# Optimization experiments

Hardware: AMD Instinct MI355X
Metric: run time of the kernel (lower is better)

## Reference

```python
import jax, jax.numpy as jnp
import numpy as np

HID = 1          # hidden_size
LAYERS = 10      # num_layers
SCALE = 60.0     # range_adjusted


def _lstm_cell(x, h, c, W_ih, W_hh, b):
    # x: [B, in], h/c: [B, HID], W_ih: [4*HID, in], W_hh: [4*HID, HID], b: [4*HID]
    g = x @ W_ih.T + h @ W_hh.T + b  # [B, 4*HID], torch gate order i,f,g,o
    i = jax.nn.sigmoid(g[:, 0:HID])
    f = jax.nn.sigmoid(g[:, HID:2 * HID])
    gg = jnp.tanh(g[:, 2 * HID:3 * HID])
    o = jax.nn.sigmoid(g[:, 3 * HID:4 * HID])
    c_new = f * c + i * gg
    h_new = o * jnp.tanh(c_new)
    return h_new, c_new


def setup_inputs() -> dict:
    key = jax.random.key(0)
    ks = jax.random.split(key, 9)
    B, T, D = 4096, 512, 32
    state = jax.random.normal(ks[0], (B, T, D), jnp.float32)
    # torch LSTM init: uniform(-1/sqrt(hidden), 1/sqrt(hidden)) = uniform(-1, 1) since HID=1
    u = lambda k, shape: jax.random.uniform(k, shape, jnp.float32, -1.0, 1.0)
    W_ih0 = u(ks[1], (4 * HID, D))            # layer 0 input weights
    W_hh0 = u(ks[2], (4 * HID, HID))
    b0 = u(ks[3], (4 * HID,)) + u(ks[4], (4 * HID,))  # b_ih + b_hh fused
    W_ih_r = u(ks[5], (LAYERS - 1, 4 * HID, HID))      # layers 1..9 input size = HID
    W_hh_r = u(ks[6], (LAYERS - 1, 4 * HID, HID))
    b_r = u(ks[7], (LAYERS - 1, 4 * HID)) + u(ks[8], (LAYERS - 1, 4 * HID))
    return {"state": state, "W_ih0": W_ih0, "W_hh0": W_hh0, "b0": b0,
            "W_ih_r": W_ih_r, "W_hh_r": W_hh_r, "b_r": b_r}


def reference(state, W_ih0, W_hh0, b0, W_ih_r, W_hh_r, b_r):
    B, T, D = state.shape
    h0 = jnp.zeros((LAYERS, B, HID), state.dtype)
    c0 = jnp.zeros_like(h0)

    def step(carry, x_t):  # x_t: [B, D]
        h, c = carry
        hs, cs = [], []
        hh, cc = _lstm_cell(x_t, h[0], c[0], W_ih0, W_hh0, b0)
        hs.append(hh); cs.append(cc)
        for l in range(LAYERS - 1):  # fixed small layer loop
            hh, cc = _lstm_cell(hh, h[l + 1], c[l + 1], W_ih_r[l], W_hh_r[l], b_r[l])
            hs.append(hh); cs.append(cc)
        return (jnp.stack(hs), jnp.stack(cs)), hh  # hh: top-layer output [B, HID]

    _, ys = jax.lax.scan(step, (h0, c0), jnp.swapaxes(state, 0, 1))  # ys: [T, B, HID]
    lstm_out = jnp.swapaxes(ys, 0, 1)  # [B, T, HID]
    return jax.nn.sigmoid(lstm_out) * SCALE
```

## Files before the change

kernel.cpp:

```cpp
#include <hip/hip_runtime.h>

#define BB 4096
#define TT 512
#define DD 32
#define NL 10
#define PH 8
#define PHASES 66

static constexpr float L2E = 1.4426950408889634f;

typedef float f4 __attribute__((ext_vector_type(4)));

__device__ __forceinline__ float fexp2(float x) { return __builtin_amdgcn_exp2f(x); }
__device__ __forceinline__ float frcp(float x)  { return __builtin_amdgcn_rcpf(x); }
__device__ __forceinline__ float fmed3(float x, float a, float b) {
    return __builtin_amdgcn_fmed3f(x, a, b);
}

__device__ __forceinline__ float dpp_shr1(float x) {
    int r = __builtin_amdgcn_update_dpp(0, __float_as_int(x), 0x111, 0xF, 0xF, true);
    return __int_as_float(r);
}

template<int CTRL>
__device__ __forceinline__ float dpp_add(float x) {
    return x + __int_as_float(__builtin_amdgcn_update_dpp(
        0, __float_as_int(x), CTRL, 0xF, 0xF, true));
}
#define DPP_XOR1 0xB1
#define DPP_XOR2 0x4E
#define DPP_ROR4 0x124

__global__ __launch_bounds__(64) void k_fused(
    const float* __restrict__ x, const float* __restrict__ Wih0,
    const float* __restrict__ Whh0, const float* __restrict__ b0,
    const float* __restrict__ Wihr, const float* __restrict__ Whhr,
    const float* __restrict__ br, float* __restrict__ out)
{
    __shared__ float4 gbuf[2][4][PH + 1];

    const int lane = threadIdx.x & 63;
    const int blk  = blockIdx.x;

    const int pg = lane >> 3;
    const int pc = lane & 7;
    const f4 pw0 = *(const f4*)(Wih0 + 0 * DD + pc * 4);
    const f4 pw1 = *(const f4*)(Wih0 + 1 * DD + pc * 4);
    const f4 pw2 = *(const f4*)(Wih0 + 2 * DD + pc * 4);
    const f4 pw3 = *(const f4*)(Wih0 + 3 * DD + pc * 4);
    const float pb0 = b0[0], pb1 = b0[1], pb2 = b0[2], pb3 = b0[3];

    const int cidx = lane >> 4;
    const int l = lane & 15;
    const int chain = blk * 4 + cidx;
    const float sk0 = -L2E, sk1 = -L2E, sk2 = -2.f * L2E, sk3 = -L2E;
    const bool isl0 = (l == 0), isl9 = (l == NL - 1);
    const int li = (l >= 1 && l <= 9) ? (l - 1) : 0;

    float wi0 = 0, wi1 = 0, wi2 = 0, wi3 = 0;
    float wh0, wh1, wh2, wh3;
    float bb0 = 0, bb1 = 0, bb2 = 0, bb3 = 0;
    if (isl0) {
        wh0 = sk0 * Whh0[0]; wh1 = sk1 * Whh0[1];
        wh2 = sk2 * Whh0[2]; wh3 = sk3 * Whh0[3];
    } else {
        const float* pi = Wihr + li * 4;
        const float* ph = Whhr + li * 4;
        const float* pb = br   + li * 4;
        wi0 = sk0 * pi[0]; wi1 = sk1 * pi[1]; wi2 = sk2 * pi[2]; wi3 = sk3 * pi[3];
        wh0 = sk0 * ph[0]; wh1 = sk1 * ph[1]; wh2 = sk2 * ph[2]; wh3 = sk3 * ph[3];
        bb0 = sk0 * pb[0]; bb1 = sk1 * pb[1]; bb2 = sk2 * pb[2]; bb3 = sk3 * pb[3];
    }

    float* outp = out + (size_t)chain * TT;
    const float c2 = 2.f * L2E;
    float h = 0.f, cs = 0.f;
    float o0 = 0.f, o1 = 0.f, o2 = 0.f, o3 = 0.f;

    const float* xb = x + (size_t)blk * 4 * TT * DD;

    f4 VA0, VA1, VA2, VA3, VB0, VB1, VB2, VB3;

    auto LOADV = [&](f4& v0, f4& v1, f4& v2, f4& v3, int p) {
        int t = p * PH + pg; t = t < TT ? t : TT - 1;
        const float* base = xb + (size_t)t * DD + pc * 4;
        v0 = __builtin_nontemporal_load((const f4*)(base + 0 * TT * DD));
        v1 = __builtin_nontemporal_load((const f4*)(base + 1 * TT * DD));
        v2 = __builtin_nontemporal_load((const f4*)(base + 2 * TT * DD));
        v3 = __builtin_nontemporal_load((const f4*)(base + 3 * TT * DD));
    };

    auto PROD1 = [&](const f4 v, int ci, int slot) {
        float p0 = v.x * pw0.x + v.y * pw0.y + v.z * pw0.z + v.w * pw0.w;
        float p1 = v.x * pw1.x + v.y * pw1.y + v.z * pw1.z + v.w * pw1.w;
        float p2 = v.x * pw2.x + v.y * pw2.y + v.z * pw2.z + v.w * pw2.w;
        float p3 = v.x * pw3.x + v.y * pw3.y + v.z * pw3.z + v.w * pw3.w;
        p0 = dpp_add<DPP_XOR1>(p0); p1 = dpp_add<DPP_XOR1>(p1);
        p2 = dpp_add<DPP_XOR1>(p2); p3 = dpp_add<DPP_XOR1>(p3);
        p0 = dpp_add<DPP_XOR2>(p0); p1 = dpp_add<DPP_XOR2>(p1);
        p2 = dpp_add<DPP_XOR2>(p2); p3 = dpp_add<DPP_XOR2>(p3);
        p0 = dpp_add<DPP_ROR4>(p0); p1 = dpp_add<DPP_ROR4>(p1);
        p2 = dpp_add<DPP_ROR4>(p2); p3 = dpp_add<DPP_ROR4>(p3);
        if (pc == 0) {
            float4 o;
            o.x = -L2E * (p0 + pb0);
            o.y = -L2E * (p1 + pb1);
            o.z = -2.f * L2E * (p2 + pb2);
            o.w = -L2E * (p3 + pb3);
            gbuf[slot][ci][pg] = o;
        }
    };

    auto READR = [&](float4* R, int slot) {
        if (isl0) {
#pragma unroll
            for (int j = 0; j < PH; j++) R[j] = gbuf[slot][cidx][j];
        }
    };

    auto STEP = [&](float4 g, int s, int jm) {
        int t = s - l;
        bool active = (t >= 0) && (t < TT);

        float hin = dpp_shr1(h);
        float u0 = fmaf(h, wh0, fmaf(hin, wi0, g.x));
        float u1 = fmaf(h, wh1, fmaf(hin, wi1, g.y));
        float u2 = fmaf(h, wh2, fmaf(hin, wi2, g.z));
        float u3 = fmaf(h, wh3, fmaf(hin, wi3, g.w));

        float E0 = fexp2(u0), E1 = fexp2(u1), E2 = fexp2(u2), E3 = fexp2(u3);
        float A0 = 1.f + E0, A1 = 1.f + E1, A2 = 1.f + E2, A3 = 1.f + E3;
        float q02  = frcp(A0 * A2);
        float num2 = fmaf(E2, c2, -c2);
        float term = num2 * q02;
        float r1   = frcp(A1);
        float csn  = fmaf(cs, r1, term);
        csn = fmed3(csn, -88.f, 88.f);
        float Ec  = fexp2(csn);
        float Ac  = 1.f + Ec;
        float qc3 = frcp(Ac * A3);
        float hn  = (1.f - Ec) * qc3;

        if (active) { cs = csn; h = hn; }

        if (jm == 1) o0 = hn;
        else if (jm == 2) o1 = hn;
        else if (jm == 3) o2 = hn;
        else o3 = hn;
        if (jm == 0 && s >= 12 && s <= 520 && isl9) {
            float4 v;
            v.x = 60.f * frcp(1.f + fexp2(-L2E * o0));
            v.y = 60.f * frcp(1.f + fexp2(-L2E * o1));
            v.z = 60.f * frcp(1.f + fexp2(-L2E * o2));
            v.w = 60.f * frcp(1.f + fexp2(-L2E * o3));
            *(float4*)(outp + (s - 12)) = v;
        }
    };

    float4 RA[PH], RB[PH];
    float4 bbv = make_float4(bb0, bb1, bb2, bb3);
#pragma unroll
    for (int i = 0; i < PH; i++) { RA[i] = bbv; RB[i] = bbv; }

    LOADV(VA0, VA1, VA2, VA3, 0);
    LOADV(VB0, VB1, VB2, VB3, 1);
    PROD1(VA0, 0, 0); PROD1(VA1, 1, 0); PROD1(VA2, 2, 0); PROD1(VA3, 3, 0);
    READR(RA, 0);
    LOADV(VA0, VA1, VA2, VA3, 2);

    for (int p = 0; p < PHASES; p += 2) {
        PROD1(VB0, 0, 1); PROD1(VB1, 1, 1); PROD1(VB2, 2, 1); PROD1(VB3, 3, 1);
#pragma unroll
        for (int j = 0; j < PH; j++) STEP(RA[j], p * PH + j, j & 3);
        READR(RB, 1);
        LOADV(VB0, VB1, VB2, VB3, p + 3);

        PROD1(VA0, 0, 0); PROD1(VA1, 1, 0); PROD1(VA2, 2, 0); PROD1(VA3, 3, 0);
#pragma unroll
        for (int j = 0; j < PH; j++) STEP(RB[j], (p + 1) * PH + j, j & 3);
        READR(RA, 0);
        LOADV(VA0, VA1, VA2, VA3, p + 4);
    }
}

extern "C" void kernel_launch(void* const* d_in, const int* in_sizes, int n_in,
                              void* d_out, int out_size, void* d_ws, size_t ws_size,
                              hipStream_t stream)
{
    const float* x    = (const float*)d_in[0];
    const float* Wih0 = (const float*)d_in[1];
    const float* Whh0 = (const float*)d_in[2];
    const float* b0   = (const float*)d_in[3];
    const float* Wihr = (const float*)d_in[4];
    const float* Whhr = (const float*)d_in[5];
    const float* br   = (const float*)d_in[6];
    float* out = (float*)d_out;

    k_fused<<<BB / 4, 64, 0, stream>>>(x, Wih0, Whh0, b0, Wihr, Whhr, br, out);
}
```

Before: 91.23 us.

## Split producer and recurrence into separate waves with LDS ring handshake

The single-wave kernel that both loaded and projected inputs and ran the 10-layer recurrence becomes a warp-specialized kernel. A producer wave does the loads and layer-0 input projections into a 4-slot LDS ring, and a consumer wave runs the serial LSTM steps. The two waves sync through volatile shared counters with s_sleep spin loops. The aim is to take memory latency and projection ALU work off the serial recurrence's critical path, at the cost of doubling the block's wave count and adding polling overhead.

```diff
diff --git a/kernel.cpp b/kernel.cpp
--- a/kernel.cpp
+++ b/kernel.cpp
@@ -6,6 +6,9 @@
 #define NL 10
 #define PH 8
 #define PHASES 66
+#define PPH 68
+#define RING 4
+#define CPB 4
 
 static constexpr float L2E = 1.4426950408889634f;
 
@@ -31,155 +34,190 @@
 #define DPP_XOR2 0x4E
 #define DPP_ROR4 0x124
 
-__global__ __launch_bounds__(64) void k_fused(
+__global__ __launch_bounds__(128) void k_fused(
     const float* __restrict__ x, const float* __restrict__ Wih0,
     const float* __restrict__ Whh0, const float* __restrict__ b0,
     const float* __restrict__ Wihr, const float* __restrict__ Whhr,
     const float* __restrict__ br, float* __restrict__ out)
 {
-    __shared__ float4 gbuf[2][4][PH + 1];
-
-    const int lane = threadIdx.x & 63;
+    __shared__ float4 gbuf[RING][CPB][PH + 1];
+    __shared__ int prod_ct;
+    __shared__ int cons_ct;
+
+    const int tid  = threadIdx.x;
+    const int wave = tid >> 6;
+    const int lane = tid & 63;
     const int blk  = blockIdx.x;
 
-    const int pg = lane >> 3;
-    const int pc = lane & 7;
-    const f4 pw0 = *(const f4*)(Wih0 + 0 * DD + pc * 4);
-    const f4 pw1 = *(const f4*)(Wih0 + 1 * DD + pc * 4);
-    const f4 pw2 = *(const f4*)(Wih0 + 2 * DD + pc * 4);
-    const f4 pw3 = *(const f4*)(Wih0 + 3 * DD + pc * 4);
-    const float pb0 = b0[0], pb1 = b0[1], pb2 = b0[2], pb3 = b0[3];
-
-    const int cidx = lane >> 4;
-    const int l = lane & 15;
-    const int chain = blk * 4 + cidx;
-    const float sk0 = -L2E, sk1 = -L2E, sk2 = -2.f * L2E, sk3 = -L2E;
-    const bool isl0 = (l == 0), isl9 = (l == NL - 1);
-    const int li = (l >= 1 && l <= 9) ? (l - 1) : 0;
-
-    float wi0 = 0, wi1 = 0, wi2 = 0, wi3 = 0;
-    float wh0, wh1, wh2, wh3;
-    float bb0 = 0, bb1 = 0, bb2 = 0, bb3 = 0;
-    if (isl0) {
-        wh0 = sk0 * Whh0[0]; wh1 = sk1 * Whh0[1];
-        wh2 = sk2 * Whh0[2]; wh3 = sk3 * Whh0[3];
+    if (tid == 0) { prod_ct = 0; cons_ct = 0; }
+    __syncthreads();
+
+    volatile int* vprod = &prod_ct;
+    volatile int* vcons = &cons_ct;
+
+    if (wave == 1) {
+        const int pg = lane >> 3;
+        const int pc = lane & 7;
+        const f4 pw0 = *(const f4*)(Wih0 + 0 * DD + pc * 4);
+        const f4 pw1 = *(const f4*)(Wih0 + 1 * DD + pc * 4);
+        const f4 pw2 = *(const f4*)(Wih0 + 2 * DD + pc * 4);
+        const f4 pw3 = *(const f4*)(Wih0 + 3 * DD + pc * 4);
+        const float pb0 = b0[0], pb1 = b0[1], pb2 = b0[2], pb3 = b0[3];
+        const float* xb = x + (size_t)blk * CPB * TT * DD;
+
+        f4 VA0, VA1, VA2, VA3, VB0, VB1, VB2, VB3;
+
+        auto LOADV = [&](f4& v0, f4& v1, f4& v2, f4& v3, int p) {
+            int t = p * PH + pg; t = t < TT ? t : TT - 1;
+            const float* base = xb + (size_t)t * DD + pc * 4;
+            v0 = __builtin_nontemporal_load((const f4*)(base + 0 * TT * DD));
+            v1 = __builtin_nontemporal_load((const f4*)(base + 1 * TT * DD));
+            v2 = __builtin_nontemporal_load((const f4*)(base + 2 * TT * DD));
+            v3 = __builtin_nontemporal_load((const f4*)(base + 3 * TT * DD));
+        };
+
+        auto PROD1 = [&](const f4 v, int ci, int slot) {
+            float p0 = v.x * pw0.x + v.y * pw0.y + v.z * pw0.z + v.w * pw0.w;
+            float p1 = v.x * pw1.x + v.y * pw1.y + v.z * pw1.z + v.w * pw1.w;
+            float p2 = v.x * pw2.x + v.y * pw2.y + v.z * pw2.z + v.w * pw2.w;
+            float p3 = v.x * pw3.x + v.y * pw3.y + v.z * pw3.z + v.w * pw3.w;
+            p0 = dpp_add<DPP_XOR1>(p0); p1 = dpp_add<DPP_XOR1>(p1);
+            p2 = dpp_add<DPP_XOR1>(p2); p3 = dpp_add<DPP_XOR1>(p3);
+            p0 = dpp_add<DPP_XOR2>(p0); p1 = dpp_add<DPP_XOR2>(p1);
+            p2 = dpp_add<DPP_XOR2>(p2); p3 = dpp_add<DPP_XOR2>(p3);
+            p0 = dpp_add<DPP_ROR4>(p0); p1 = dpp_add<DPP_ROR4>(p1);
+            p2 = dpp_add<DPP_ROR4>(p2); p3 = dpp_add<DPP_ROR4>(p3);
+            if (pc == 0) {
+                float4 o;
+                o.x = -L2E * (p0 + pb0);
+                o.y = -L2E * (p1 + pb1);
+                o.z = -2.f * L2E * (p2 + pb2);
+                o.w = -L2E * (p3 + pb3);
+                gbuf[slot][ci][pg] = o;
+            }
+        };
+
+        auto waitcons = [&](int v) {
+            while (*vcons < v) __builtin_amdgcn_s_sleep(8);
+        };
+
+        LOADV(VA0, VA1, VA2, VA3, 0);
+        for (int q = 0; q < PPH; q += 2) {
+            LOADV(VB0, VB1, VB2, VB3, q + 1);
+            waitcons(q - (RING - 1));
+            PROD1(VA0, 0, q & 3); PROD1(VA1, 1, q & 3);
+            PROD1(VA2, 2, q & 3); PROD1(VA3, 3, q & 3);
+            asm volatile("s_waitcnt lgkmcnt(0)" ::: "memory");
+            if (lane == 0) *vprod = q + 1;
+            if (q + 2 < PPH) LOADV(VA0, VA1, VA2, VA3, q + 2);
+            waitcons(q + 1 - (RING - 1));
+            PROD1(VB0, 0, (q + 1) & 3); PROD1(VB1, 1, (q + 1) & 3);
+            PROD1(VB2, 2, (q + 1) & 3); PROD1(VB3, 3, (q + 1) & 3);
+            asm volatile("s_waitcnt lgkmcnt(0)" ::: "memory");
+            if (lane == 0) *vprod = q + 2;
+        }
     } else {
-        const float* pi = Wihr + li * 4;
-        const float* ph = Whhr + li * 4;
-        const float* pb = br   + li * 4;
-        wi0 = sk0 * pi[0]; wi1 = sk1 * pi[1]; wi2 = sk2 * pi[2]; wi3 = sk3 * pi[3];
-        wh0 = sk0 * ph[0]; wh1 = sk1 * ph[1]; wh2 = sk2 * ph[2]; wh3 = sk3 * ph[3];
-        bb0 = sk0 * pb[0]; bb1 = sk1 * pb[1]; bb2 = sk2 * pb[2]; bb3 = sk3 * pb[3];
-    }
-
-    float* outp = out + (size_t)chain * TT;
-    const float c2 = 2.f * L2E;
-    float h = 0.f, cs = 0.f;
-    float o0 = 0.f, o1 = 0.f, o2 = 0.f, o3 = 0.f;
-
-    const float* xb = x + (size_t)blk * 4 * TT * DD;
-
-    f4 VA0, VA1, VA2, VA3, VB0, VB1, VB2, VB3;
-
-    auto LOADV = [&](f4& v0, f4& v1, f4& v2, f4& v3, int p) {
-        int t = p * PH + pg; t = t < TT ? t : TT - 1;
-        const float* base = xb + (size_t)t * DD + pc * 4;
-        v0 = __builtin_nontemporal_load((const f4*)(base + 0 * TT * DD));
-        v1 = __builtin_nontemporal_load((const f4*)(base + 1 * TT * DD));
-        v2 = __builtin_nontemporal_load((const f4*)(base + 2 * TT * DD));
-        v3 = __builtin_nontemporal_load((const f4*)(base + 3 * TT * DD));
-    };
-
-    auto PROD1 = [&](const f4 v, int ci, int slot) {
-        float p0 = v.x * pw0.x + v.y * pw0.y + v.z * pw0.z + v.w * pw0.w;
-        float p1 = v.x * pw1.x + v.y * pw1.y + v.z * pw1.z + v.w * pw1.w;
-        float p2 = v.x * pw2.x + v.y * pw2.y + v.z * pw2.z + v.w * pw2.w;
-        float p3 = v.x * pw3.x + v.y * pw3.y + v.z * pw3.z + v.w * pw3.w;
-        p0 = dpp_add<DPP_XOR1>(p0); p1 = dpp_add<DPP_XOR1>(p1);
-        p2 = dpp_add<DPP_XOR1>(p2); p3 = dpp_add<DPP_XOR1>(p3);
-        p0 = dpp_add<DPP_XOR2>(p0); p1 = dpp_add<DPP_XOR2>(p1);
-        p2 = dpp_add<DPP_XOR2>(p2); p3 = dpp_add<DPP_XOR2>(p3);
-        p0 = dpp_add<DPP_ROR4>(p0); p1 = dpp_add<DPP_ROR4>(p1);
-        p2 = dpp_add<DPP_ROR4>(p2); p3 = dpp_add<DPP_ROR4>(p3);
-        if (pc == 0) {
-            float4 o;
-            o.x = -L2E * (p0 + pb0);
-            o.y = -L2E * (p1 + pb1);
-            o.z = -2.f * L2E * (p2 + pb2);
-            o.w = -L2E * (p3 + pb3);
-            gbuf[slot][ci][pg] = o;
+        const int cidx = lane >> 4;
+        const int l = lane & 15;
+        const int chain = blk * CPB + cidx;
+        const float sk0 = -L2E, sk1 = -L2E, sk2 = -2.f * L2E, sk3 = -L2E;
+        const bool isl0 = (l == 0), isl9 = (l == NL - 1);
+        const int li = (l >= 1 && l <= 9) ? (l - 1) : 0;
+
+        float wi0 = 0, wi1 = 0, wi2 = 0, wi3 = 0;
+        float wh0, wh1, wh2, wh3;
+        float bb0 = 0, bb1 = 0, bb2 = 0, bb3 = 0;
+        if (isl0) {
+            wh0 = sk0 * Whh0[0]; wh1 = sk1 * Whh0[1];
+            wh2 = sk2 * Whh0[2]; wh3 = sk3 * Whh0[3];
+        } else {
+            const float* pi = Wihr + li * 4;
+            const float* ph = Whhr + li * 4;
+            const float* pb = br   + li * 4;
+            wi0 = sk0 * pi[0]; wi1 = sk1 * pi[1]; wi2 = sk2 * pi[2]; wi3 = sk3 * pi[3];
+            wh0 = sk0 * ph[0]; wh1 = sk1 * ph[1]; wh2 = sk2 * ph[2]; wh3 = sk3 * ph[3];
+            bb0 = sk0 * pb[0]; bb1 = sk1 * pb[1]; bb2 = sk2 * pb[2]; bb3 = sk3 * pb[3];
         }
-    };
-
-    auto READR = [&](float4* R, int slot) {
-        if (isl0) {
-#pragma unroll
-            for (int j = 0; j < PH; j++) R[j] = gbuf[slot][cidx][j];
+
+        float* outp = out + (size_t)chain * TT;
+        const float c2 = 2.f * L2E;
+        float h = 0.f, cs = 0.f;
+        float o0 = 0.f, o1 = 0.f, o2 = 0.f, o3 = 0.f;
+
+        auto READR = [&](float4* R, int slot) {
+            if (isl0) {
+#pragma unroll
+                for (int j = 0; j < PH; j++) R[j] = gbuf[slot][cidx][j];
+            }
+        };
+
+        auto waitprod = [&](int v) {
+            while (*vprod < v) __builtin_amdgcn_s_sleep(1);
+        };
+
+        auto STEP = [&](float4 g, int s, int jm) {
+            int t = s - l;
+            bool active = (t >= 0) && (t < TT);
+
+            float hin = dpp_shr1(h);
+            float u0 = fmaf(h, wh0, fmaf(hin, wi0, g.x));
+            float u1 = fmaf(h, wh1, fmaf(hin, wi1, g.y));
+            float u2 = fmaf(h, wh2, fmaf(hin, wi2, g.z));
+            float u3 = fmaf(h, wh3, fmaf(hin, wi3, g.w));
+
+            float E0 = fexp2(u0), E1 = fexp2(u1), E2 = fexp2(u2), E3 = fexp2(u3);
+            float A0 = 1.f + E0, A1 = 1.f + E1, A2 = 1.f + E2, A3 = 1.f + E3;
+            float q02  = frcp(A0 * A2);
+            float num2 = fmaf(E2, c2, -c2);
+            float term = num2 * q02;
+            float r1   = frcp(A1);
+            float csn  = fmaf(cs, r1, term);
+            csn = fmed3(csn, -88.f, 88.f);
+            float Ec  = fexp2(csn);
+            float Ac  = 1.f + Ec;
+            float qc3 = frcp(Ac * A3);
+            float hn  = (1.f - Ec) * qc3;
+
+            if (active) { cs = csn; h = hn; }
+
+            if (jm == 1) o0 = hn;
+            else if (jm == 2) o1 = hn;
+            else if (jm == 3) o2 = hn;
+            else o3 = hn;
+            if (jm == 0 && s >= 12 && s <= 520 && isl9) {
+                float4 v;
+                v.x = 60.f * frcp(1.f + fexp2(-L2E * o0));
+                v.y = 60.f * frcp(1.f + fexp2(-L2E * o1));
+                v.z = 60.f * frcp(1.f + fexp2(-L2E * o2));
+                v.w = 60.f * frcp(1.f + fexp2(-L2E * o3));
+                *(float4*)(outp + (s - 12)) = v;
+            }
+        };
+
+        float4 RA[PH], RB[PH];
+        float4 bbv = make_float4(bb0, bb1, bb2, bb3);
+#pragma unroll
+        for (int i = 0; i < PH; i++) { RA[i] = bbv; RB[i] = bbv; }
+
+        waitprod(1);
+        READR(RA, 0);
+        asm volatile("s_waitcnt lgkmcnt(0)" ::: "memory");
+        if (lane == 0) *vcons = 1;
+
+        for (int p = 0; p < PHASES; p += 2) {
+#pragma unroll
+            for (int j = 0; j < PH; j++) STEP(RA[j], p * PH + j, j & 3);
+            waitprod(p + 2);
+            READR(RB, (p + 1) & 3);
+            asm volatile("s_waitcnt lgkmcnt(0)" ::: "memory");
+            if (lane == 0) *vcons = p + 2;
+#pragma unroll
+            for (int j = 0; j < PH; j++) STEP(RB[j], (p + 1) * PH + j, j & 3);
+            waitprod(p + 3);
+            READR(RA, (p + 2) & 3);
+            asm volatile("s_waitcnt lgkmcnt(0)" ::: "memory");
+            if (lane == 0) *vcons = p + 3;
         }
-    };
-
-    auto STEP = [&](float4 g, int s, int jm) {
-        int t = s - l;
-        bool active = (t >= 0) && (t < TT);
-
-        float hin = dpp_shr1(h);
-        float u0 = fmaf(h, wh0, fmaf(hin, wi0, g.x));
-        float u1 = fmaf(h, wh1, fmaf(hin, wi1, g.y));
-        float u2 = fmaf(h, wh2, fmaf(hin, wi2, g.z));
-        float u3 = fmaf(h, wh3, fmaf(hin, wi3, g.w));
-
-        float E0 = fexp2(u0), E1 = fexp2(u1), E2 = fexp2(u2), E3 = fexp2(u3);
-        float A0 = 1.f + E0, A1 = 1.f + E1, A2 = 1.f + E2, A3 = 1.f + E3;
-        float q02  = frcp(A0 * A2);
-        float num2 = fmaf(E2, c2, -c2);
-        float term = num2 * q02;
-        float r1   = frcp(A1);
-        float csn  = fmaf(cs, r1, term);
-        csn = fmed3(csn, -88.f, 88.f);
-        float Ec  = fexp2(csn);
-        float Ac  = 1.f + Ec;
-        float qc3 = frcp(Ac * A3);
-        float hn  = (1.f - Ec) * qc3;
-
-        if (active) { cs = csn; h = hn; }
-
-        if (jm == 1) o0 = hn;
-        else if (jm == 2) o1 = hn;
-        else if (jm == 3) o2 = hn;
-        else o3 = hn;
-        if (jm == 0 && s >= 12 && s <= 520 && isl9) {
-            float4 v;
-            v.x = 60.f * frcp(1.f + fexp2(-L2E * o0));
-            v.y = 60.f * frcp(1.f + fexp2(-L2E * o1));
-            v.z = 60.f * frcp(1.f + fexp2(-L2E * o2));
-            v.w = 60.f * frcp(1.f + fexp2(-L2E * o3));
-            *(float4*)(outp + (s - 12)) = v;
-        }
-    };
-
-    float4 RA[PH], RB[PH];
-    float4 bbv = make_float4(bb0, bb1, bb2, bb3);
-#pragma unroll
-    for (int i = 0; i < PH; i++) { RA[i] = bbv; RB[i] = bbv; }
-
-    LOADV(VA0, VA1, VA2, VA3, 0);
-    LOADV(VB0, VB1, VB2, VB3, 1);
-    PROD1(VA0, 0, 0); PROD1(VA1, 1, 0); PROD1(VA2, 2, 0); PROD1(VA3, 3, 0);
-    READR(RA, 0);
-    LOADV(VA0, VA1, VA2, VA3, 2);
-
-    for (int p = 0; p < PHASES; p += 2) {
-        PROD1(VB0, 0, 1); PROD1(VB1, 1, 1); PROD1(VB2, 2, 1); PROD1(VB3, 3, 1);
-#pragma unroll
-        for (int j = 0; j < PH; j++) STEP(RA[j], p * PH + j, j & 3);
-        READR(RB, 1);
-        LOADV(VB0, VB1, VB2, VB3, p + 3);
-
-        PROD1(VA0, 0, 0); PROD1(VA1, 1, 0); PROD1(VA2, 2, 0); PROD1(VA3, 3, 0);
-#pragma unroll
-        for (int j = 0; j < PH; j++) STEP(RB[j], (p + 1) * PH + j, j & 3);
-        READR(RA, 0);
-        LOADV(VA0, VA1, VA2, VA3, p + 4);
     }
 }
 
@@ -196,5 +234,5 @@
     const float* br   = (const float*)d_in[6];
     float* out = (float*)d_out;
 
-    k_fused<<<BB / 4, 64, 0, stream>>>(x, Wih0, Whh0, b0, Wihr, Whhr, br, out);
-}
+    k_fused<<<BB / CPB, 128, 0, stream>>>(x, Wih0, Whh0, b0, Wihr, Whhr, br, out);
+}
```

Result: slower. 104.1 us (+14.2%).
